# Optimization experiments

Hardware: AMD Instinct MI355X
Metric: run time of the kernel (lower is better)

Reference implementation:

```python
import jax, jax.numpy as jnp
import numpy as np

EPS = 1e-5

def layer_norm(x, g, b):
    mu = jnp.mean(x, axis=-1, keepdims=True)
    var = jnp.mean(jnp.square(x - mu), axis=-1, keepdims=True)
    return (x - mu) * jax.lax.rsqrt(var + EPS) * g + b

def gather_recent(seq_tokens, seq_mask, count):
    # vectorized right-aligned gather of last `count` valid tokens per row
    B, S, D = seq_tokens.shape
    csum = jnp.cumsum(seq_mask.astype(jnp.int32), axis=1)          # [B,S]
    total = csum[:, -1:]                                           # [B,1]
    rank = total - csum                                            # 0 = last valid (at valid positions)
    sel = seq_mask & (rank < count)
    dest = jnp.where(sel, count - 1 - rank, count)                 # dump invalid into slot `count`
    b_idx = jnp.arange(B)[:, None]
    buf = jnp.zeros((B, count + 1, D), seq_tokens.dtype)
    recent = buf.at[b_idx, dest].set(seq_tokens * sel[..., None].astype(seq_tokens.dtype))[:, :count]
    recent_mask = jnp.arange(count)[None, :] >= (count - total)    # [B,count]
    return recent, recent_mask

def setup_inputs() -> dict:
    key = jax.random.key(0)
    B, S, D, H, P = 16, 2048, 1024, 16, 8
    ks = jax.random.split(key, 8)
    hidden_states = jax.random.normal(ks[0], (B, S, D), jnp.float32)
    lengths = jax.random.randint(ks[1], (B,), 1, S + 1)
    valid_mask = jnp.arange(S)[None, :] < lengths[:, None]
    s = 0.02
    return {
        "hidden_states": hidden_states,
        "valid_mask": valid_mask,
        "queries": jax.random.normal(ks[2], (P, D), jnp.float32) * s,
        "in_proj_w": jax.random.normal(ks[3], (3 * D, D), jnp.float32) * s,
        "in_proj_b": jnp.zeros((3 * D,), jnp.float32),
        "out_w": jax.random.normal(ks[4], (D, D), jnp.float32) * s,
        "out_b": jnp.zeros((D,), jnp.float32),
        "ln_pma_g": jnp.ones((D,), jnp.float32),
        "ln_pma_b": jnp.zeros((D,), jnp.float32),
        "ln_v_g": jnp.ones((D,), jnp.float32),
        "ln_v_b": jnp.zeros((D,), jnp.float32),
        "W_v": jax.random.normal(ks[5], (D, D), jnp.float32) * s,
        "b_v": jnp.zeros((D,), jnp.float32),
        "ln_g_g": jnp.ones((D,), jnp.float32),
        "ln_g_b": jnp.zeros((D,), jnp.float32),
        "W_g": jax.random.normal(ks[6], (D, D), jnp.float32) * s,
        "b_g": jnp.zeros((D,), jnp.float32),
        "cls_count": 1, "pma_count": 8, "recent_count": 64, "num_heads": 16,
    }

def reference(hidden_states, valid_mask, queries, in_proj_w, in_proj_b, out_w, out_b,
              ln_pma_g, ln_pma_b, ln_v_g, ln_v_b, W_v, b_v, ln_g_g, ln_g_b, W_g, b_g,
              cls_count, pma_count, recent_count, num_heads):
    B, S, D = hidden_states.shape
    H = num_heads
    hd = D // H
    # ---- PMA (torch nn.MultiheadAttention, batch_first, eval/no-dropout) ----
    Wq, Wk, Wv_ = in_proj_w[:D], in_proj_w[D:2 * D], in_proj_w[2 * D:]
    bq, bk, bv_ = in_proj_b[:D], in_proj_b[D:2 * D], in_proj_b[2 * D:]
    q = (queries @ Wq.T + bq)                       # [P, D]
    k = hidden_states @ Wk.T + bk                   # [B, S, D]
    v = hidden_states @ Wv_.T + bv_                 # [B, S, D]
    qh = q.reshape(pma_count, H, hd)                # [P, H, hd]
    kh = k.reshape(B, S, H, hd)
    vh = v.reshape(B, S, H, hd)
    scores = jnp.einsum('phd,bshd->bhps', qh, kh) / jnp.sqrt(jnp.asarray(hd, hidden_states.dtype))
    scores = jnp.where(valid_mask[:, None, None, :], scores, jnp.asarray(-1e9, scores.dtype))
    attn = jax.nn.softmax(scores, axis=-1)          # [B, H, P, S]
    ctx = jnp.einsum('bhps,bshd->bphd', attn, vh).reshape(B, pma_count, D)
    pooled = ctx @ out_w.T + out_b
    pma_tokens = layer_norm(queries[None, :, :] + pooled, ln_pma_g, ln_pma_b)  # [B, P, D]
    pma_mask = jnp.ones((B, pma_count), bool)
    # ---- split cls / sequence, gather recent ----
    cls_tokens = hidden_states[:, :cls_count]
    cls_mask = valid_mask[:, :cls_count]
    recent_tokens, recent_mask = gather_recent(hidden_states[:, cls_count:],
                                               valid_mask[:, cls_count:], recent_count)
    summary = jnp.concatenate([cls_tokens, pma_tokens, recent_tokens], axis=1)
    summary_mask = jnp.concatenate([cls_mask, pma_mask, recent_mask], axis=1)
    # ---- SiLU self-gating ----
    val = jax.nn.silu(layer_norm(summary, ln_v_g, ln_v_b) @ W_v.T + b_v)
    gate = jax.nn.sigmoid(layer_norm(summary, ln_g_g, ln_g_b) @ W_g.T + b_g)
    gated = gate * val * summary_mask[..., None].astype(summary.dtype)
    return gated, summary_mask
```

## Files before the change

kernel.cpp:

```cpp
#include <hip/hip_runtime.h>
#include <hip/hip_bf16.h>
#include <math.h>


#define Bn 16
#define Sn 2048
#define Dn 1024
#define Hn 16
#define Pn 8
#define Tn 73
#define RECn 64
#define UPITCH 520

typedef __attribute__((ext_vector_type(8))) short short8;
typedef __attribute__((ext_vector_type(4))) float f32x4;

__device__ __forceinline__ short f2bf(float x) {
    union { __hip_bfloat16 h; short s; } u;
    u.h = __float2bfloat16(x);
    return u.s;
}
__device__ __forceinline__ float bf2f(short s) {
    return __uint_as_float(((unsigned)(unsigned short)s) << 16);
}

__device__ __forceinline__ bool mask_at(const void* raw, int f, size_t idx) {
    return f ? (((const unsigned char*)raw)[idx] != 0)
             : (((const int*)raw)[idx] != 0);
}

__device__ __forceinline__ void gload_lds16(const void* g, void* l) {
    __builtin_amdgcn_global_load_lds((const __attribute__((address_space(1))) void*)g,
                                     (__attribute__((address_space(3))) void*)l, 16, 0, 0);
}

__global__ __launch_bounds__(256) void setup1_kernel(const float* __restrict__ queries,
                                                     const float* __restrict__ in_w,
                                                     const float* __restrict__ in_b,
                                                     const unsigned char* __restrict__ raw,
                                                     float* __restrict__ q,
                                                     int* __restrict__ flag) {
    if (blockIdx.x == 2048) {
        __shared__ int any;
        if (threadIdx.x == 0) any = 0;
        __syncthreads();
        const uint4* r4 = (const uint4*)raw;
        int local = 0;
        for (int i = threadIdx.x; i < (Bn * Sn) / 16; i += blockDim.x) {
            uint4 w = r4[i];
            if ((w.x & 0xFFFFFF00u) | (w.y & 0xFFFFFF00u) |
                (w.z & 0xFFFFFF00u) | (w.w & 0xFFFFFF00u)) local = 1;
        }
        if (local) any = 1;
        __syncthreads();
        if (threadIdx.x == 0) *flag = any;
        return;
    }
    int wid = (blockIdx.x * blockDim.x + threadIdx.x) >> 6;
    int lane = threadIdx.x & 63;
    if (wid >= Pn * Dn) return;
    int p = wid >> 10, j = wid & 1023;
    float acc = 0.0f;
    for (int c = lane; c < Dn; c += 64)
        acc += queries[p * Dn + c] * in_w[(size_t)j * Dn + c];
#pragma unroll
    for (int off = 32; off > 0; off >>= 1) acc += __shfl_down(acc, off);
    if (lane == 0) q[wid] = acc + in_b[j];
}

__global__ __launch_bounds__(256) void setup2_kernel(const float* __restrict__ q,
                                                     const float* __restrict__ in_w,
                                                     const float* __restrict__ in_b,
                                                     const void* __restrict__ raw,
                                                     const int* __restrict__ flag,
                                                     short* __restrict__ Atile,
                                                     float* __restrict__ c0,
                                                     int* __restrict__ totals,
                                                     int* __restrict__ rsrc,
                                                     float* __restrict__ maskf) {
    __shared__ float qs[8][64];
    __shared__ int lc[256];
    if (blockIdx.x < 64) {
        int h = blockIdx.x >> 2, cblk = blockIdx.x & 3;
        int c = cblk * 256 + threadIdx.x;
        for (int i = threadIdx.x; i < 512; i += 256) {
            int p = i >> 6, d = i & 63;
            qs[p][d] = q[p * Dn + h * 64 + d];
        }
        __syncthreads();
        float acc[8] = {};
#pragma unroll 8
        for (int d = 0; d < 64; d++) {
            float w = in_w[(size_t)(Dn + h * 64 + d) * Dn + c];
#pragma unroll
            for (int p = 0; p < 8; p++) acc[p] = fmaf(qs[p][d], w, acc[p]);
        }
        int kc = c >> 5, kq = (c >> 3) & 3, e = c & 7;
#pragma unroll
        for (int p = 0; p < 8; p++) {
            int hp = h * 8 + p;
            int slot = hp * 4 + (kq ^ ((hp >> 1) & 3));
            Atile[(size_t)kc * 4096 + slot * 8 + e] = f2bf(acc[p] * 0.125f);
        }
        if (cblk == 0 && threadIdx.x < 8) {
            int p = threadIdx.x;
            float a = 0.0f;
            for (int d = 0; d < 64; d++) a += qs[p][d] * in_b[Dn + h * 64 + d];
            c0[h * 8 + p] = a * 0.125f;
        }
        return;
    }
    int b = blockIdx.x - 64, t = threadIdx.x;
    int f = *flag;
    const int SP = Sn - 1;
    if (t < RECn) rsrc[b * RECn + t] = -1;
    int base = t * 8;
    unsigned char m[8];
    int cnt = 0;
#pragma unroll
    for (int i = 0; i < 8; i++) {
        int idx = base + i;
        m[i] = (idx < SP) ? (mask_at(raw, f, (size_t)b * Sn + 1 + idx) ? 1 : 0) : 0;
        cnt += m[i];
    }
    lc[t] = cnt;
    __syncthreads();
    for (int off = 1; off < 256; off <<= 1) {
        int add = (t >= off) ? lc[t - off] : 0;
        __syncthreads();
        lc[t] += add;
        __syncthreads();
    }
    int total = lc[255];
    int run = lc[t] - cnt;
#pragma unroll
    for (int i = 0; i < 8; i++) {
        if (m[i]) {
            run++;
            int rank = total - run;
            if (rank < RECn) rsrc[b * RECn + (RECn - 1 - rank)] = base + i + 1;
        }
    }
    if (t == 0) totals[b] = total;
    if (t < Tn) {
        float mv;
        if (t == 0) mv = mask_at(raw, f, (size_t)b * Sn) ? 1.0f : 0.0f;
        else if (t < 1 + Pn) mv = 1.0f;
        else mv = ((t - 9) >= RECn - total) ? 1.0f : 0.0f;
        maskf[b * Tn + t] = mv;
    }
}

__global__ __launch_bounds__(256) void scores_mfma(const float* __restrict__ hidden,
                                                   const short* __restrict__ Atile,
                                                   const float* __restrict__ c0,
                                                   const void* __restrict__ raw,
                                                   const int* __restrict__ flag,
                                                   float* __restrict__ scores) {
    __shared__ float Af[2][32 * 32];
    __shared__ short Bs[2][128 * 32];
    int tid = threadIdx.x, wave = tid >> 6, lane = tid & 63;
    int l15 = lane & 15, q = lane >> 4;
    int m0 = blockIdx.x * 32;
    int b = m0 >> 11, s_base = m0 & 2047;
    int ws = wave >> 1, wh = wave & 1;
    int s0 = ws * 16, hp0 = wh * 64;

    auto stage = [&](int bb, int k0) {
        {
            int s = tid >> 3, j = (tid & 7) ^ (s & 7);
            gload_lds16(hidden + (size_t)(m0 + s) * Dn + k0 + j * 4, &Af[bb][tid * 4]);
        }
        const short* src = Atile + (size_t)(k0 >> 5) * 4096;
#pragma unroll
        for (int u = 0; u < 2; u++) {
            int i = tid + u * 256;
            gload_lds16(src + i * 8, &Bs[bb][i * 8]);
        }
    };

    f32x4 acc[4] = {};
    stage(0, 0);
    __syncthreads();

    for (int t = 0; t < 32; t++) {
        int bb = t & 1;
        if (t + 1 < 32) stage(bb ^ 1, (t + 1) * 32);
        short8 av;
        {
            int s = s0 + l15;
            int base = s * 8;
            f32x4 lo = *(const f32x4*)&Af[bb][(base + ((2 * q) ^ (s & 7))) * 4];
            f32x4 hi = *(const f32x4*)&Af[bb][(base + ((2 * q + 1) ^ (s & 7))) * 4];
#pragma unroll
            for (int i = 0; i < 4; i++) { av[i] = f2bf(lo[i]); av[i + 4] = f2bf(hi[i]); }
        }
#pragma unroll
        for (int f = 0; f < 4; f++) {
            int hp = hp0 + f * 16 + l15;
            short8 bv = *(const short8*)&Bs[bb][(hp * 4 + (q ^ ((hp >> 1) & 3))) * 8];
            acc[f] = __builtin_amdgcn_mfma_f32_16x16x32_bf16(av, bv, acc[f], 0, 0, 0);
        }
        __syncthreads();
    }

    int fl = *flag;
    int srow = s_base + s0 + q * 4;
    size_t vbase = (size_t)b * Sn + srow;
    bool ok0 = mask_at(raw, fl, vbase), ok1 = mask_at(raw, fl, vbase + 1);
    bool ok2 = mask_at(raw, fl, vbase + 2), ok3 = mask_at(raw, fl, vbase + 3);
#pragma unroll
    for (int f = 0; f < 4; f++) {
        int hp = hp0 + f * 16 + l15;
        float cc = c0[hp];
        f32x4 st;
        st[0] = ok0 ? acc[f][0] + cc : -1.0e9f;
        st[1] = ok1 ? acc[f][1] + cc : -1.0e9f;
        st[2] = ok2 ? acc[f][2] + cc : -1.0e9f;
        st[3] = ok3 ? acc[f][3] + cc : -1.0e9f;
        *(f32x4*)(scores + (size_t)(b * 128 + hp) * Sn + srow) = st;
    }
}

__global__ __launch_bounds__(256) void softmax_kernel(const float* __restrict__ scores,
                                                      short* __restrict__ attn_bf) {
    const float* row = scores + (size_t)blockIdx.x * Sn;
    short* orow = attn_bf + (size_t)blockIdx.x * Sn;
    int t = threadIdx.x;
    __shared__ float red[256];
    f32x4 v0 = *(const f32x4*)(row + t * 8);
    f32x4 v1 = *(const f32x4*)(row + t * 8 + 4);
    float mx = -1.0e30f;
#pragma unroll
    for (int i = 0; i < 4; i++) { mx = fmaxf(mx, v0[i]); mx = fmaxf(mx, v1[i]); }
    red[t] = mx;
    __syncthreads();
    for (int off = 128; off > 0; off >>= 1) {
        if (t < off) red[t] = fmaxf(red[t], red[t + off]);
        __syncthreads();
    }
    mx = red[0];
    __syncthreads();
    float e[8];
    float sum = 0.0f;
#pragma unroll
    for (int i = 0; i < 4; i++) {
        e[i] = expf(v0[i] - mx); sum += e[i];
        e[i + 4] = expf(v1[i] - mx); sum += e[i + 4];
    }
    red[t] = sum;
    __syncthreads();
    for (int off = 128; off > 0; off >>= 1) {
        if (t < off) red[t] += red[t + off];
        __syncthreads();
    }
    float inv = 1.0f / red[0];
    short8 o;
#pragma unroll
    for (int i = 0; i < 8; i++) o[i] = f2bf(e[i] * inv);
    *(short8*)(orow + t * 8) = o;
}

__global__ __launch_bounds__(512) void U_mfma(const short* __restrict__ attn_bf,
                                              const float* __restrict__ hidden,
                                              short* __restrict__ Up0,
                                              short* __restrict__ Up1,
                                              short* __restrict__ Up2,
                                              short* __restrict__ Up3) {
    __shared__ short Hs[64 * UPITCH];
    int n0 = blockIdx.x * 64, b = blockIdx.y, z = blockIdx.z;
    int zbase = z * 512;
    short* Up = (z == 0) ? Up0 : (z == 1) ? Up1 : (z == 2) ? Up2 : Up3;
    int tid = threadIdx.x, wave = tid >> 6, lane = tid & 63;
    int l15 = lane & 15, q = lane >> 4;

    {
        int slot = tid & 15, rgrp = tid >> 4;
        const float* srcb = hidden + ((size_t)b * Sn + zbase) * Dn + n0 + slot * 4;
#pragma unroll
        for (int p = 0; p < 16; p++) {
            int row = p * 32 + rgrp;
            f32x4 v = *(const f32x4*)(srcb + (size_t)row * Dn);
#pragma unroll
            for (int i = 0; i < 4; i++) {
                int c = slot * 4 + i;
                Hs[c * UPITCH + (row ^ ((c & 7) << 3))] = f2bf(v[i]);
            }
        }
    }
    __syncthreads();

    const short* ap = attn_bf + ((size_t)b * 128 + wave * 16 + l15) * Sn + zbase + q * 8;
    f32x4 acc[4] = {};
    short8 pa4[4];
#pragma unroll
    for (int d = 0; d < 4; d++) pa4[d] = *(const short8*)(ap + d * 32);
#pragma unroll
    for (int ic = 0; ic < 16; ic++) {
        short8 av = pa4[ic & 3];
        if (ic + 4 < 16) pa4[ic & 3] = *(const short8*)(ap + (ic + 4) * 32);
#pragma unroll
        for (int nf = 0; nf < 4; nf++) {
            int c = nf * 16 + l15;
            int ks = (ic * 32 + q * 8) ^ ((c & 7) << 3);
            short8 bv = *(const short8*)(&Hs[c * UPITCH + ks]);
            acc[nf] = __builtin_amdgcn_mfma_f32_16x16x32_bf16(av, bv, acc[nf], 0, 0, 0);
        }
    }
    int hp = wave * 16 + q * 4;
#pragma unroll
    for (int nf = 0; nf < 4; nf++) {
        int c = n0 + nf * 16 + l15;
        short* up = Up + (size_t)(b * 128 + hp) * Dn + c;
#pragma unroll
        for (int r = 0; r < 4; r++) up[(size_t)r * Dn] = f2bf(acc[nf][r]);
    }
}

__global__ __launch_bounds__(64) void ctx_mfma(const short* __restrict__ Up0,
                                               const short* __restrict__ Up1,
                                               const short* __restrict__ Up2,
                                               const short* __restrict__ Up3,
                                               const float* __restrict__ in_w,
                                               const float* __restrict__ in_b,
                                               float* __restrict__ ctx) {
    int bh = blockIdx.x, b = bh >> 4, h = bh & 15;
    int lane = threadIdx.x & 63, l15 = lane & 15, koff = (lane >> 4) * 8;
    int p = l15 & 7;
    size_t uoff = ((size_t)b * 128 + h * 8 + p) * Dn + koff;
    const float* wv = in_w + (size_t)(2 * Dn + h * 64 + l15) * Dn + koff;
    f32x4 acc[4] = {};
    for (int k0 = 0; k0 < Dn; k0 += 32) {
        short8 s0 = *(const short8*)(Up0 + uoff + k0);
        short8 s1 = *(const short8*)(Up1 + uoff + k0);
        short8 s2 = *(const short8*)(Up2 + uoff + k0);
        short8 s3 = *(const short8*)(Up3 + uoff + k0);
        short8 av;
#pragma unroll
        for (int i = 0; i < 8; i++)
            av[i] = f2bf((bf2f(s0[i]) + bf2f(s1[i])) + (bf2f(s2[i]) + bf2f(s3[i])));
#pragma unroll
        for (int nt = 0; nt < 4; nt++) {
            f32x4 w0 = *(const f32x4*)(wv + (size_t)nt * 16 * Dn + k0);
            f32x4 w1 = *(const f32x4*)(wv + (size_t)nt * 16 * Dn + k0 + 4);
            short8 bv;
#pragma unroll
            for (int i = 0; i < 4; i++) { bv[i] = f2bf(w0[i]); bv[i + 4] = f2bf(w1[i]); }
            acc[nt] = __builtin_amdgcn_mfma_f32_16x16x32_bf16(av, bv, acc[nt], 0, 0, 0);
        }
    }
    if (lane < 32) {
        int prow = (lane >> 4) * 4;
#pragma unroll
        for (int nt = 0; nt < 4; nt++) {
            int d = h * 64 + nt * 16 + l15;
            float bias = in_b[2 * Dn + d];
#pragma unroll
            for (int r = 0; r < 4; r++)
                ctx[(size_t)(b * 8 + prow + r) * Dn + d] = acc[nt][r] + bias;
        }
    }
}

__global__ __launch_bounds__(256) void pooled_mfma(const float* __restrict__ A,
                                                   const float* __restrict__ B,
                                                   const float* __restrict__ bias,
                                                   float* __restrict__ C, int M) {
    int wave = threadIdx.x >> 6, lane = threadIdx.x & 63;
    int l15 = lane & 15, koff = (lane >> 4) * 8;
    int m0 = blockIdx.x * 64 + (wave >> 1) * 32;
    int n0 = blockIdx.y * 64 + (wave & 1) * 32;
    f32x4 acc[2][2] = {};
    int ra0 = min(m0 + l15, M - 1);
    int ra1 = min(m0 + 16 + l15, M - 1);
    const float* a0p = A + (size_t)ra0 * Dn + koff;
    const float* a1p = A + (size_t)ra1 * Dn + koff;
    const float* b0p = B + (size_t)(n0 + l15) * Dn + koff;
    const float* b1p = B + (size_t)(n0 + 16 + l15) * Dn + koff;
    for (int k0 = 0; k0 < Dn; k0 += 32) {
        short8 av0, av1, bv0, bv1;
        f32x4 x, y;
        x = *(const f32x4*)(a0p + k0); y = *(const f32x4*)(a0p + k0 + 4);
#pragma unroll
        for (int i = 0; i < 4; i++) { av0[i] = f2bf(x[i]); av0[i + 4] = f2bf(y[i]); }
        x = *(const f32x4*)(a1p + k0); y = *(const f32x4*)(a1p + k0 + 4);
#pragma unroll
        for (int i = 0; i < 4; i++) { av1[i] = f2bf(x[i]); av1[i + 4] = f2bf(y[i]); }
        x = *(const f32x4*)(b0p + k0); y = *(const f32x4*)(b0p + k0 + 4);
#pragma unroll
        for (int i = 0; i < 4; i++) { bv0[i] = f2bf(x[i]); bv0[i + 4] = f2bf(y[i]); }
        x = *(const f32x4*)(b1p + k0); y = *(const f32x4*)(b1p + k0 + 4);
#pragma unroll
        for (int i = 0; i < 4; i++) { bv1[i] = f2bf(x[i]); bv1[i + 4] = f2bf(y[i]); }
        acc[0][0] = __builtin_amdgcn_mfma_f32_16x16x32_bf16(av0, bv0, acc[0][0], 0, 0, 0);
        acc[0][1] = __builtin_amdgcn_mfma_f32_16x16x32_bf16(av0, bv1, acc[0][1], 0, 0, 0);
        acc[1][0] = __builtin_amdgcn_mfma_f32_16x16x32_bf16(av1, bv0, acc[1][0], 0, 0, 0);
        acc[1][1] = __builtin_amdgcn_mfma_f32_16x16x32_bf16(av1, bv1, acc[1][1], 0, 0, 0);
    }
#pragma unroll
    for (int mf = 0; mf < 2; mf++) {
        int row0 = m0 + mf * 16 + (lane >> 4) * 4;
#pragma unroll
        for (int nf = 0; nf < 2; nf++) {
            int col = n0 + nf * 16 + l15;
            float bval = bias[col];
#pragma unroll
            for (int r = 0; r < 4; r++) {
                int row = row0 + r;
                if (row < M) C[(size_t)row * Dn + col] = acc[mf][nf][r] + bval;
            }
        }
    }
}

__global__ __launch_bounds__(256) void wgemm_mfma(const short* __restrict__ lnv,
                                                  const short* __restrict__ lng,
                                                  const float* __restrict__ Wv,
                                                  const float* __restrict__ Wg,
                                                  const float* __restrict__ bv_,
                                                  const float* __restrict__ bg_,
                                                  float* __restrict__ c1,
                                                  float* __restrict__ c2, int M) {
    int z = blockIdx.z;
    const short* Abf = z ? lng : lnv;
    const float* Bw = z ? Wg : Wv;
    const float* bias = z ? bg_ : bv_;
    float* C = z ? c2 : c1;
    int wave = threadIdx.x >> 6, lane = threadIdx.x & 63;
    int l15 = lane & 15, koff = (lane >> 4) * 8;
    int m0 = blockIdx.x * 64 + (wave >> 1) * 32;
    int n0 = blockIdx.y * 64 + (wave & 1) * 32;
    f32x4 acc[2][2] = {};
    int ra0 = min(m0 + l15, M - 1);
    int ra1 = min(m0 + 16 + l15, M - 1);
    const short* a0p = Abf + (size_t)ra0 * Dn + koff;
    const short* a1p = Abf + (size_t)ra1 * Dn + koff;
    const float* b0p = Bw + (size_t)(n0 + l15) * Dn + koff;
    const float* b1p = Bw + (size_t)(n0 + 16 + l15) * Dn + koff;
    for (int k0 = 0; k0 < Dn; k0 += 32) {
        short8 av0 = *(const short8*)(a0p + k0);
        short8 av1 = *(const short8*)(a1p + k0);
        short8 bv0, bv1;
        f32x4 x, y;
        x = *(const f32x4*)(b0p + k0); y = *(const f32x4*)(b0p + k0 + 4);
#pragma unroll
        for (int i = 0; i < 4; i++) { bv0[i] = f2bf(x[i]); bv0[i + 4] = f2bf(y[i]); }
        x = *(const f32x4*)(b1p + k0); y = *(const f32x4*)(b1p + k0 + 4);
#pragma unroll
        for (int i = 0; i < 4; i++) { bv1[i] = f2bf(x[i]); bv1[i + 4] = f2bf(y[i]); }
        acc[0][0] = __builtin_amdgcn_mfma_f32_16x16x32_bf16(av0, bv0, acc[0][0], 0, 0, 0);
        acc[0][1] = __builtin_amdgcn_mfma_f32_16x16x32_bf16(av0, bv1, acc[0][1], 0, 0, 0);
        acc[1][0] = __builtin_amdgcn_mfma_f32_16x16x32_bf16(av1, bv0, acc[1][0], 0, 0, 0);
        acc[1][1] = __builtin_amdgcn_mfma_f32_16x16x32_bf16(av1, bv1, acc[1][1], 0, 0, 0);
    }
#pragma unroll
    for (int mf = 0; mf < 2; mf++) {
        int row0 = m0 + mf * 16 + (lane >> 4) * 4;
#pragma unroll
        for (int nf = 0; nf < 2; nf++) {
            int col = n0 + nf * 16 + l15;
            float bval = bias[col];
#pragma unroll
            for (int r = 0; r < 4; r++) {
                int row = row0 + r;
                if (row < M) C[(size_t)row * Dn + col] = acc[mf][nf][r] + bval;
            }
        }
    }
}

__device__ __forceinline__ float block_sum(float v, float* red) {
    int tid = threadIdx.x;
    red[tid] = v;
    __syncthreads();
    for (int off = 128; off > 0; off >>= 1) {
        if (tid < off) red[tid] += red[tid + off];
        __syncthreads();
    }
    float r = red[0];
    __syncthreads();
    return r;
}

__global__ void summary_ln_kernel(const float* __restrict__ hidden,
                                  const float* __restrict__ queries,
                                  const float* __restrict__ pooled,
                                  const int* __restrict__ rsrc,
                                  const float* __restrict__ gpma, const float* __restrict__ bpma,
                                  const float* __restrict__ gv, const float* __restrict__ bv,
                                  const float* __restrict__ gg, const float* __restrict__ bg,
                                  short* __restrict__ lnv, short* __restrict__ lng) {
    __shared__ float red[256];
    int b = blockIdx.x, t = blockIdx.y, tid = threadIdx.x;
    float x[4];
    if (t == 0) {
#pragma unroll
        for (int i = 0; i < 4; i++)
            x[i] = hidden[(size_t)b * Sn * Dn + tid + i * 256];
    } else if (t < 1 + Pn) {
        int p = t - 1;
#pragma unroll
        for (int i = 0; i < 4; i++) {
            int c = tid + i * 256;
            x[i] = queries[p * Dn + c] + pooled[((size_t)b * Pn + p) * Dn + c];
        }
    } else {
        int src = rsrc[b * RECn + (t - 9)];
        if (src >= 0) {
#pragma unroll
            for (int i = 0; i < 4; i++)
                x[i] = hidden[((size_t)b * Sn + src) * Dn + tid + i * 256];
        } else {
#pragma unroll
            for (int i = 0; i < 4; i++) x[i] = 0.0f;
        }
    }
    if (t >= 1 && t < 1 + Pn) {
        float mu = block_sum(x[0] + x[1] + x[2] + x[3], red) * (1.0f / Dn);
        float d2 = 0.0f;
#pragma unroll
        for (int i = 0; i < 4; i++) { float d = x[i] - mu; d2 += d * d; }
        float inv = rsqrtf(block_sum(d2, red) * (1.0f / Dn) + 1e-5f);
#pragma unroll
        for (int i = 0; i < 4; i++) {
            int c = tid + i * 256;
            x[i] = (x[i] - mu) * inv * gpma[c] + bpma[c];
        }
    }
    float mu = block_sum(x[0] + x[1] + x[2] + x[3], red) * (1.0f / Dn);
    float d2 = 0.0f;
#pragma unroll
    for (int i = 0; i < 4; i++) { float d = x[i] - mu; d2 += d * d; }
    float inv = rsqrtf(block_sum(d2, red) * (1.0f / Dn) + 1e-5f);
    size_t row = (size_t)(b * Tn + t) * Dn;
#pragma unroll
    for (int i = 0; i < 4; i++) {
        int c = tid + i * 256;
        float xh = (x[i] - mu) * inv;
        lnv[row + c] = f2bf(xh * gv[c] + bv[c]);
        lng[row + c] = f2bf(xh * gg[c] + bg[c]);
    }
}

__global__ void gated_kernel(const float* __restrict__ c1, const float* __restrict__ c2,
                             const float* __restrict__ maskf, float* __restrict__ out) {
    int gi = blockIdx.x * blockDim.x + threadIdx.x;
    int row = gi >> 10;
    float m = maskf[row];
    float a = c1[gi], g = c2[gi];
    float sv = a / (1.0f + expf(-a));
    float sg = 1.0f / (1.0f + expf(-g));
    out[gi] = sg * sv * m;
}

extern "C" void kernel_launch(void* const* d_in, const int* in_sizes, int n_in,
                              void* d_out, int out_size, void* d_ws, size_t ws_size,
                              hipStream_t stream) {
    const float* hidden = (const float*)d_in[0];
    const void* valid_raw = d_in[1];
    const float* queries = (const float*)d_in[2];
    const float* in_w = (const float*)d_in[3];
    const float* in_b = (const float*)d_in[4];
    const float* out_w = (const float*)d_in[5];
    const float* out_b = (const float*)d_in[6];
    const float* ln_pma_g = (const float*)d_in[7];
    const float* ln_pma_b = (const float*)d_in[8];
    const float* ln_v_g = (const float*)d_in[9];
    const float* ln_v_b = (const float*)d_in[10];
    const float* W_v = (const float*)d_in[11];
    const float* b_v = (const float*)d_in[12];
    const float* ln_g_g = (const float*)d_in[13];
    const float* ln_g_b = (const float*)d_in[14];
    const float* W_g = (const float*)d_in[15];
    const float* b_g = (const float*)d_in[16];

    float* ws = (float*)d_ws;
    float* out = (float*)d_out;

    float* SC      = ws;
    short* attn_bf = (short*)(ws + 4194304);
    short* Up0     = (short*)ws;
    short* Up1     = (short*)(ws + 1048576);
    short* Up2     = (short*)(ws + 2097152);
    short* Up3     = (short*)(ws + 3145728);
    float* qbuf    = ws + 10485760;
    short* Atile   = (short*)(ws + 10493952);
    float* c0      = ws + 10559488;
    float* ctx     = ws + 10559744;
    float* pooled  = ws + 10690816;
    int*   ivals   = (int*)(ws + 11870464);
    int* totals = ivals;
    int* rsrc = ivals + 16;
    int* flag = ivals + 16 + 1024;
    short* lnv_bf = (short*)ws;
    short* lng_bf = (short*)(ws + 622592);
    float* c1 = ws + 1245184;
    float* c2 = ws + 2441216;
    float* maskf = out + (size_t)Bn * Tn * Dn;

    const int M2 = Bn * Tn;

    setup1_kernel<<<2049, 256, 0, stream>>>(queries, in_w, in_b,
                                            (const unsigned char*)valid_raw, qbuf, flag);
    setup2_kernel<<<80, 256, 0, stream>>>(qbuf, in_w, in_b, valid_raw, flag,
                                          Atile, c0, totals, rsrc, maskf);
    scores_mfma<<<(Bn * Sn) / 32, 256, 0, stream>>>(hidden, Atile, c0, valid_raw, flag, SC);
    softmax_kernel<<<Bn * 128, 256, 0, stream>>>(SC, attn_bf);
    U_mfma<<<dim3(16, Bn, 4), 512, 0, stream>>>(attn_bf, hidden, Up0, Up1, Up2, Up3);
    ctx_mfma<<<Bn * Hn, 64, 0, stream>>>(Up0, Up1, Up2, Up3, in_w, in_b, ctx);
    pooled_mfma<<<dim3(2, 16), 256, 0, stream>>>(ctx, out_w, out_b, pooled, Bn * Pn);
    summary_ln_kernel<<<dim3(Bn, Tn), 256, 0, stream>>>(hidden, queries, pooled, rsrc,
                                                        ln_pma_g, ln_pma_b, ln_v_g, ln_v_b,
                                                        ln_g_g, ln_g_b, lnv_bf, lng_bf);
    wgemm_mfma<<<dim3((M2 + 63) / 64, 16, 2), 256, 0, stream>>>(lnv_bf, lng_bf, W_v, W_g,
                                                                b_v, b_g, c1, c2, M2);
    gated_kernel<<<(Bn * Tn * Dn) / 256, 256, 0, stream>>>(c1, c2, maskf, out);
}
```

Measured before the change: 232.3 us.

## Drop LDS staging in scores kernel; load operands directly to registers per wave

The scores GEMM no longer stages hidden and the projected-query tile through double-buffered LDS with block barriers. Each wave now owns 16 rows and all 128 head-query columns, reading A straight from global memory and B from a new MFMA-fragment-ordered layout written by setup2, with register-level prefetch of the next K chunk. This removes the LDS traffic and __syncthreads, but raises register use (8 accumulators plus two sets of 8 B fragments) and makes every wave re-read the full B tile from global/L2.

```diff
diff --git a/kernel.cpp b/kernel.cpp
--- a/kernel.cpp
+++ b/kernel.cpp
@@ -27,11 +27,6 @@
 __device__ __forceinline__ bool mask_at(const void* raw, int f, size_t idx) {
     return f ? (((const unsigned char*)raw)[idx] != 0)
              : (((const int*)raw)[idx] != 0);
-}
-
-__device__ __forceinline__ void gload_lds16(const void* g, void* l) {
-    __builtin_amdgcn_global_load_lds((const __attribute__((address_space(1))) void*)g,
-                                     (__attribute__((address_space(3))) void*)l, 16, 0, 0);
 }
 
 __global__ __launch_bounds__(256) void setup1_kernel(const float* __restrict__ queries,
@@ -73,7 +68,7 @@
                                                      const float* __restrict__ in_b,
                                                      const void* __restrict__ raw,
                                                      const int* __restrict__ flag,
-                                                     short* __restrict__ Atile,
+                                                     short* __restrict__ Btile,
                                                      float* __restrict__ c0,
                                                      int* __restrict__ totals,
                                                      int* __restrict__ rsrc,
@@ -99,8 +94,8 @@
 #pragma unroll
         for (int p = 0; p < 8; p++) {
             int hp = h * 8 + p;
-            int slot = hp * 4 + (kq ^ ((hp >> 1) & 3));
-            Atile[(size_t)kc * 4096 + slot * 8 + e] = f2bf(acc[p] * 0.125f);
+            size_t slot = (size_t)(kc * 8 + (hp >> 4)) * 64 + kq * 16 + (hp & 15);
+            Btile[slot * 8 + e] = f2bf(acc[p] * 0.125f);
         }
         if (cblk == 0 && threadIdx.x < 8) {
             int p = threadIdx.x;
@@ -152,72 +147,61 @@
 }
 
 __global__ __launch_bounds__(256) void scores_mfma(const float* __restrict__ hidden,
-                                                   const short* __restrict__ Atile,
+                                                   const short* __restrict__ Btile,
                                                    const float* __restrict__ c0,
                                                    const void* __restrict__ raw,
                                                    const int* __restrict__ flag,
                                                    float* __restrict__ scores) {
-    __shared__ float Af[2][32 * 32];
-    __shared__ short Bs[2][128 * 32];
     int tid = threadIdx.x, wave = tid >> 6, lane = tid & 63;
     int l15 = lane & 15, q = lane >> 4;
-    int m0 = blockIdx.x * 32;
+    int m0 = blockIdx.x * 64 + wave * 16;
     int b = m0 >> 11, s_base = m0 & 2047;
-    int ws = wave >> 1, wh = wave & 1;
-    int s0 = ws * 16, hp0 = wh * 64;
-
-    auto stage = [&](int bb, int k0) {
-        {
-            int s = tid >> 3, j = (tid & 7) ^ (s & 7);
-            gload_lds16(hidden + (size_t)(m0 + s) * Dn + k0 + j * 4, &Af[bb][tid * 4]);
-        }
-        const short* src = Atile + (size_t)(k0 >> 5) * 4096;
-#pragma unroll
-        for (int u = 0; u < 2; u++) {
-            int i = tid + u * 256;
-            gload_lds16(src + i * 8, &Bs[bb][i * 8]);
-        }
-    };
-
-    f32x4 acc[4] = {};
-    stage(0, 0);
-    __syncthreads();
-
-    for (int t = 0; t < 32; t++) {
-        int bb = t & 1;
-        if (t + 1 < 32) stage(bb ^ 1, (t + 1) * 32);
+
+    const float* aptr = hidden + (size_t)(m0 + l15) * Dn + q * 8;
+    const short* bbase = Btile + (size_t)lane * 8;
+
+    f32x4 acc[8] = {};
+    short8 bcur[8], bnxt[8];
+    f32x4 a0c = *(const f32x4*)(aptr);
+    f32x4 a1c = *(const f32x4*)(aptr + 4);
+    f32x4 a0n, a1n;
+#pragma unroll
+    for (int nt = 0; nt < 8; nt++)
+        bcur[nt] = *(const short8*)(bbase + (size_t)nt * 512);
+
+    for (int kc = 0; kc < 32; kc++) {
+        if (kc + 1 < 32) {
+#pragma unroll
+            for (int nt = 0; nt < 8; nt++)
+                bnxt[nt] = *(const short8*)(bbase + (size_t)((kc + 1) * 8 + nt) * 512);
+            a0n = *(const f32x4*)(aptr + (kc + 1) * 32);
+            a1n = *(const f32x4*)(aptr + (kc + 1) * 32 + 4);
+        }
         short8 av;
-        {
-            int s = s0 + l15;
-            int base = s * 8;
-            f32x4 lo = *(const f32x4*)&Af[bb][(base + ((2 * q) ^ (s & 7))) * 4];
-            f32x4 hi = *(const f32x4*)&Af[bb][(base + ((2 * q + 1) ^ (s & 7))) * 4];
-#pragma unroll
-            for (int i = 0; i < 4; i++) { av[i] = f2bf(lo[i]); av[i + 4] = f2bf(hi[i]); }
-        }
-#pragma unroll
-        for (int f = 0; f < 4; f++) {
-            int hp = hp0 + f * 16 + l15;
-            short8 bv = *(const short8*)&Bs[bb][(hp * 4 + (q ^ ((hp >> 1) & 3))) * 8];
-            acc[f] = __builtin_amdgcn_mfma_f32_16x16x32_bf16(av, bv, acc[f], 0, 0, 0);
-        }
-        __syncthreads();
+#pragma unroll
+        for (int i = 0; i < 4; i++) { av[i] = f2bf(a0c[i]); av[i + 4] = f2bf(a1c[i]); }
+#pragma unroll
+        for (int nt = 0; nt < 8; nt++)
+            acc[nt] = __builtin_amdgcn_mfma_f32_16x16x32_bf16(av, bcur[nt], acc[nt], 0, 0, 0);
+#pragma unroll
+        for (int nt = 0; nt < 8; nt++) bcur[nt] = bnxt[nt];
+        a0c = a0n; a1c = a1n;
     }
 
     int fl = *flag;
-    int srow = s_base + s0 + q * 4;
+    int srow = s_base + q * 4;
     size_t vbase = (size_t)b * Sn + srow;
     bool ok0 = mask_at(raw, fl, vbase), ok1 = mask_at(raw, fl, vbase + 1);
     bool ok2 = mask_at(raw, fl, vbase + 2), ok3 = mask_at(raw, fl, vbase + 3);
 #pragma unroll
-    for (int f = 0; f < 4; f++) {
-        int hp = hp0 + f * 16 + l15;
+    for (int nt = 0; nt < 8; nt++) {
+        int hp = nt * 16 + l15;
         float cc = c0[hp];
         f32x4 st;
-        st[0] = ok0 ? acc[f][0] + cc : -1.0e9f;
-        st[1] = ok1 ? acc[f][1] + cc : -1.0e9f;
-        st[2] = ok2 ? acc[f][2] + cc : -1.0e9f;
-        st[3] = ok3 ? acc[f][3] + cc : -1.0e9f;
+        st[0] = ok0 ? acc[nt][0] + cc : -1.0e9f;
+        st[1] = ok1 ? acc[nt][1] + cc : -1.0e9f;
+        st[2] = ok2 ? acc[nt][2] + cc : -1.0e9f;
+        st[3] = ok3 ? acc[nt][3] + cc : -1.0e9f;
         *(f32x4*)(scores + (size_t)(b * 128 + hp) * Sn + srow) = st;
     }
 }
@@ -584,7 +568,7 @@
     short* Up2     = (short*)(ws + 2097152);
     short* Up3     = (short*)(ws + 3145728);
     float* qbuf    = ws + 10485760;
-    short* Atile   = (short*)(ws + 10493952);
+    short* Btile   = (short*)(ws + 10493952);
     float* c0      = ws + 10559488;
     float* ctx     = ws + 10559744;
     float* pooled  = ws + 10690816;
@@ -603,8 +587,8 @@
     setup1_kernel<<<2049, 256, 0, stream>>>(queries, in_w, in_b,
                                             (const unsigned char*)valid_raw, qbuf, flag);
     setup2_kernel<<<80, 256, 0, stream>>>(qbuf, in_w, in_b, valid_raw, flag,
-                                          Atile, c0, totals, rsrc, maskf);
-    scores_mfma<<<(Bn * Sn) / 32, 256, 0, stream>>>(hidden, Atile, c0, valid_raw, flag, SC);
+                                          Btile, c0, totals, rsrc, maskf);
+    scores_mfma<<<(Bn * Sn) / 64, 256, 0, stream>>>(hidden, Btile, c0, valid_raw, flag, SC);
     softmax_kernel<<<Bn * 128, 256, 0, stream>>>(SC, attn_bf);
     U_mfma<<<dim3(16, Bn, 4), 512, 0, stream>>>(attn_bf, hidden, Up0, Up1, Up2, Up3);
     ctx_mfma<<<Bn * Hn, 64, 0, stream>>>(Up0, Up1, Up2, Up3, in_w, in_b, ctx);
```

New measurement: 243.6 us. 1.05x slower.
